# Kernel tuning notes

Hardware: AMD Instinct MI355X
Metric: run time of the kernel (lower is better)

The kernel has to match this reference:

```python
import jax, jax.numpy as jnp
import numpy as np
import math

LN_EPS = 1e-5

def setup_inputs() -> dict:
    key = jax.random.key(0)
    ks = jax.random.split(key, 8)
    B, S, D = 2, 2048, 2048
    sc = 1.0 / math.sqrt(D)
    return {
        "x": jax.random.normal(ks[0], (B, S, D), dtype=jnp.float32),
        "Wq": jax.random.normal(ks[1], (D, D), dtype=jnp.float32) * sc,
        "bq": jnp.zeros((D,), jnp.float32),
        "Wk": jax.random.normal(ks[2], (D, D), dtype=jnp.float32) * sc,
        "bk": jnp.zeros((D,), jnp.float32),
        "Wv": jax.random.normal(ks[3], (D, D), dtype=jnp.float32) * sc,
        "bv": jnp.zeros((D,), jnp.float32),
        "Wo": jax.random.normal(ks[4], (D, D), dtype=jnp.float32) * sc,
        "bo": jnp.zeros((D,), jnp.float32),
        "gamma": jnp.ones((D,), jnp.float32),
        "beta": jnp.zeros((D,), jnp.float32),
        "num_heads": 16,
    }

def reference(x, Wq, bq, Wk, bk, Wv, bv, Wo, bo, gamma, beta, num_heads):
    B, S, D = x.shape
    H = num_heads
    Dh = D // H
    # projections (torch Linear: y = x W^T + b; here W stored as [in,out])
    q = (x @ Wq + bq).reshape(B, S, H, Dh).transpose(0, 2, 1, 3)  # [B,H,S,Dh]
    k = (x @ Wk + bk).reshape(B, S, H, Dh).transpose(0, 2, 1, 3)
    v = (x @ Wv + bv).reshape(B, S, H, Dh).transpose(0, 2, 1, 3)
    scores = jnp.einsum("bhqd,bhkd->bhqk", q, k) / jnp.sqrt(jnp.asarray(Dh, x.dtype))
    causal = jnp.tril(jnp.ones((S, S), bool))  # [S,S]
    scores = jnp.where(causal[None, None], scores, -jnp.inf)
    # original subtracts row-max then softmax == stable softmax
    attn = jax.nn.softmax(scores, axis=-1)
    ctx = jnp.einsum("bhqk,bhkd->bhqd", attn, v)
    ctx = ctx.transpose(0, 2, 1, 3).reshape(B, S, D)
    attn_out = ctx @ Wo + bo
    y = attn_out + x
    mu = jnp.mean(y, axis=-1, keepdims=True)
    var = jnp.mean((y - mu) ** 2, axis=-1, keepdims=True)
    ln = gamma * (y - mu) * jax.lax.rsqrt(var + LN_EPS) + beta
    return (ln, attn_out, k, v)
```

## Files before the change

kernel.cpp:

```cpp
#include <hip/hip_runtime.h>
#include <hip/hip_bf16.h>
#include <math.h>
#include <stdint.h>

typedef __bf16 bf16;
typedef __bf16 bf16x4 __attribute__((ext_vector_type(4)));
typedef __bf16 bf16x8 __attribute__((ext_vector_type(8)));
typedef float f32x4 __attribute__((ext_vector_type(4)));

#define D_MODEL 2048
#define SEQ     2048
#define NHEADS  16
#define DH      128

__device__ __forceinline__ void async_copy16(const bf16* g, bf16* l) {
    typedef const unsigned int __attribute__((address_space(1))) gu32;
    typedef unsigned int __attribute__((address_space(3))) lu32;
    __builtin_amdgcn_global_load_lds((gu32*)g, (lu32*)(unsigned int)(unsigned long long)(l),
                                     16, 0, 0);
}

__global__ __launch_bounds__(256)
void convert_x_kernel(const float* __restrict__ x, bf16* __restrict__ xb)
{
    int i = blockIdx.x * 256 + threadIdx.x;
    float4 v = ((const float4*)x)[i];
    bf16x4 o;
    o[0] = (bf16)v.x; o[1] = (bf16)v.y; o[2] = (bf16)v.z; o[3] = (bf16)v.w;
    ((bf16x4*)xb)[i] = o;
}

__global__ __launch_bounds__(256)
void transpose_w_kernel(const float* __restrict__ Wq, const float* __restrict__ Wk,
                        const float* __restrict__ Wv, const float* __restrict__ Wo,
                        bf16* __restrict__ WTbase)
{
    const int z = blockIdx.z;
    const float* __restrict__ W = (z == 0) ? Wq : (z == 1) ? Wk : (z == 2) ? Wv : Wo;
    bf16* __restrict__ Wt = WTbase + (size_t)z * (D_MODEL * D_MODEL);
    const int n0 = blockIdx.x * 64, k0 = blockIdx.y * 64;
    const int tid = threadIdx.x;
    __shared__ bf16 Tl[64][68];

#pragma unroll
    for (int i = 0; i < 4; ++i) {
        int idx = tid + i * 256;
        int kr = idx >> 4, nc = (idx & 15) * 4;
        float4 w = *(const float4*)&W[(size_t)(k0 + kr) * D_MODEL + n0 + nc];
        Tl[nc + 0][kr] = (bf16)w.x;
        Tl[nc + 1][kr] = (bf16)w.y;
        Tl[nc + 2][kr] = (bf16)w.z;
        Tl[nc + 3][kr] = (bf16)w.w;
    }
    __syncthreads();
#pragma unroll
    for (int i = 0; i < 4; ++i) {
        int idx = tid + i * 256;
        int nr = idx >> 4, kc = (idx & 15) * 4;
        *(bf16x4*)&Wt[(size_t)(n0 + nr) * D_MODEL + k0 + kc] = *(const bf16x4*)&Tl[nr][kc];
    }
}

__global__ __launch_bounds__(256)
void transpose_v_kernel(const float* __restrict__ V, bf16* __restrict__ Vt)
{
    const int s0 = blockIdx.x * 64, d0 = blockIdx.y * 64, bh = blockIdx.z;
    const float* __restrict__ Vb = V + (size_t)bh * SEQ * DH;
    bf16* __restrict__ Vtb = Vt + (size_t)bh * DH * SEQ;
    const int tid = threadIdx.x;
    __shared__ bf16 Tl[64][68];

#pragma unroll
    for (int i = 0; i < 4; ++i) {
        int idx = tid + i * 256;
        int sr = idx >> 4, dc = (idx & 15) * 4;
        float4 v = *(const float4*)&Vb[(size_t)(s0 + sr) * DH + d0 + dc];
        Tl[dc + 0][sr] = (bf16)v.x;
        Tl[dc + 1][sr] = (bf16)v.y;
        Tl[dc + 2][sr] = (bf16)v.z;
        Tl[dc + 3][sr] = (bf16)v.w;
    }
    __syncthreads();
#pragma unroll
    for (int i = 0; i < 4; ++i) {
        int idx = tid + i * 256;
        int dr = idx >> 4, sc = (idx & 15) * 4;
        *(bf16x4*)&Vtb[(size_t)(d0 + dr) * SEQ + s0 + sc] = *(const bf16x4*)&Tl[dr][sc];
    }
}

__device__ __forceinline__ void gemm128_core(const bf16* __restrict__ A,
                                             const bf16* __restrict__ Bt,
                                             int bm, int bn,
                                             int wave, int lane,
                                             bf16* As, bf16* Bs,
                                             f32x4 acc[4][4])
{
    const int l16 = lane & 15, quad = lane >> 4;
    const int wave_m = wave >> 1, wave_n = wave & 1;

    for (int k0 = 0; k0 < D_MODEL; k0 += 64) {
#pragma unroll
        for (int jj = 0; jj < 4; ++jj) {
            int j = wave * 4 + jj;
            int mt = j >> 1, kk = j & 1;
            int col = k0 + kk * 32 + quad * 8;
            const bf16* ga = &A[(size_t)(bm * 128 + mt * 16 + l16) * D_MODEL + col];
            async_copy16(ga, &As[j * 512]);
            const bf16* gb = &Bt[(size_t)(bn * 128 + mt * 16 + l16) * D_MODEL + col];
            async_copy16(gb, &Bs[j * 512]);
        }
        __syncthreads();
#pragma unroll
        for (int kk = 0; kk < 2; ++kk) {
            bf16x8 a[4], b[4];
#pragma unroll
            for (int t = 0; t < 4; ++t) {
                a[t] = *(const bf16x8*)&As[(((wave_m * 4 + t) * 2 + kk) * 64 + lane) * 8];
                b[t] = *(const bf16x8*)&Bs[(((wave_n * 4 + t) * 2 + kk) * 64 + lane) * 8];
            }
#pragma unroll
            for (int t = 0; t < 4; ++t)
#pragma unroll
                for (int t2 = 0; t2 < 4; ++t2)
                    acc[t][t2] = __builtin_amdgcn_mfma_f32_16x16x32_bf16(a[t], b[t2], acc[t][t2], 0, 0, 0);
        }
        __syncthreads();
    }
}

__global__ __launch_bounds__(256)
void gemm_qkv_kernel(const bf16* __restrict__ A, const bf16* __restrict__ WT,
                     const float* __restrict__ bq, const float* __restrict__ bk,
                     const float* __restrict__ bv,
                     bf16* __restrict__ qout, float* __restrict__ kout,
                     bf16* __restrict__ kb16, float* __restrict__ vout)
{
    const int z = blockIdx.z;
    const bf16* __restrict__ Bt = WT + (size_t)z * (D_MODEL * D_MODEL);
    const float* __restrict__ bias = (z == 0) ? bq : (z == 1) ? bk : bv;
    const int bm = blockIdx.y, bn = blockIdx.x;
    const int tid = threadIdx.x;
    const int wave = tid >> 6, lane = tid & 63, quad = lane >> 4, l16 = lane & 15;
    const int wave_m = wave >> 1, wave_n = wave & 1;

    __shared__ bf16 As[8192];
    __shared__ bf16 Bs[8192];
    f32x4 acc[4][4] = {};

    gemm128_core(A, Bt, bm, bn, wave, lane, As, Bs, acc);

#pragma unroll
    for (int t = 0; t < 4; ++t) {
#pragma unroll
        for (int t2 = 0; t2 < 4; ++t2) {
#pragma unroll
            for (int r = 0; r < 4; ++r) {
                int m = bm * 128 + wave_m * 64 + t * 16 + quad * 4 + r;
                int n = bn * 128 + wave_n * 64 + t2 * 16 + l16;
                float val = acc[t][t2][r] + bias[n];
                int b = m >> 11, s = m & (SEQ - 1);
                int h = n >> 7, dh = n & (DH - 1);
                size_t off = ((size_t)(b * NHEADS + h) * SEQ + s) * DH + dh;
                if (z == 0) {
                    qout[off] = (bf16)val;
                } else if (z == 1) {
                    kout[off] = val;
                    kb16[off] = (bf16)val;
                } else {
                    vout[off] = val;
                }
            }
        }
    }
}

__global__ __launch_bounds__(256)
void gemm_out_kernel(const bf16* __restrict__ A, const bf16* __restrict__ Bt,
                     const float* __restrict__ bias, float* __restrict__ out)
{
    const int bm = blockIdx.y, bn = blockIdx.x;
    const int tid = threadIdx.x;
    const int wave = tid >> 6, lane = tid & 63, quad = lane >> 4, l16 = lane & 15;
    const int wave_m = wave >> 1, wave_n = wave & 1;

    __shared__ bf16 As[8192];
    __shared__ bf16 Bs[8192];
    f32x4 acc[4][4] = {};

    gemm128_core(A, Bt, bm, bn, wave, lane, As, Bs, acc);

#pragma unroll
    for (int t = 0; t < 4; ++t) {
#pragma unroll
        for (int t2 = 0; t2 < 4; ++t2) {
#pragma unroll
            for (int r = 0; r < 4; ++r) {
                int m = bm * 128 + wave_m * 64 + t * 16 + quad * 4 + r;
                int n = bn * 128 + wave_n * 64 + t2 * 16 + l16;
                out[(size_t)m * D_MODEL + n] = acc[t][t2][r] + bias[n];
            }
        }
    }
}

__global__ __launch_bounds__(256, 4)
void attn_kernel(const bf16* __restrict__ Q, const bf16* __restrict__ K,
                 const bf16* __restrict__ Vt, bf16* __restrict__ ctx)
{
    const int id = blockIdx.x;
    const int p  = id & 511;
    const int bh = p >> 4;
    const int j  = p & 15;
    const int qb = (id >> 9) ? j : (31 - j);

    const int tid = threadIdx.x;
    const int wave = tid >> 6, lane = tid & 63, quad = lane >> 4, l16 = lane & 15;

    __shared__ bf16 Ks[64 * 128];
    __shared__ bf16 VsT[128 * 64];
    __shared__ bf16 Ps[4 * 16 * 64];
    char* const ksb = (char*)Ks;
    char* const vsb = (char*)VsT;
    char* const psb = (char*)Ps + wave * 2048;

    const bf16* qsrc = Q + ((size_t)bh * SEQ + (size_t)qb * 64 + wave * 16 + l16) * DH;
    bf16x8 qf[4];
#pragma unroll
    for (int dd = 0; dd < 4; ++dd)
        qf[dd] = *(const bf16x8*)&qsrc[dd * 32 + quad * 8];

    f32x4 o[8] = {};
    float m_i[4], l_i[4];
#pragma unroll
    for (int r = 0; r < 4; ++r) { m_i[r] = -INFINITY; l_i[r] = 0.f; }

    const float scale = 0.08838834764831845f;
    const bf16* ksrc0 = K + (size_t)bh * SEQ * DH;
    const bf16* vsrc0 = Vt + (size_t)bh * DH * SEQ;

    for (int kb = 0; kb <= qb; ++kb) {
        __syncthreads();

        {
            const char* kg = (const char*)(ksrc0 + (size_t)(kb * 64) * DH);
#pragma unroll
            for (int i = 0; i < 4; ++i) {
                int seg = i * 4 + wave;
                int row = seg * 4 + (lane >> 4);
                int colb = (lane & 15) * 16;
                const char* src = kg + row * 256 + (colb ^ ((row & 7) << 4));
                async_copy16((const bf16*)src, (bf16*)(ksb + seg * 1024));
            }
            const char* vg = (const char*)(vsrc0 + kb * 64);
#pragma unroll
            for (int i = 0; i < 4; ++i) {
                int seg = i * 4 + wave;
                int d = seg * 8 + (lane >> 3);
                int colb = (lane & 7) * 16;
                const char* src = vg + (size_t)d * (SEQ * 2) + (colb ^ ((d & 7) << 4));
                async_copy16((const bf16*)src, (bf16*)(vsb + seg * 1024));
            }
        }
        __syncthreads();

        float pvals[4][4];
#pragma unroll
        for (int t = 0; t < 4; ++t) {
            f32x4 s = {};
            const int row = t * 16 + l16;
            const int swz = (row & 7) << 4;
#pragma unroll
            for (int dd = 0; dd < 4; ++dd) {
                bf16x8 b = *(const bf16x8*)(ksb + row * 256 + ((dd * 64 + quad * 16) ^ swz));
                s = __builtin_amdgcn_mfma_f32_16x16x32_bf16(qf[dd], b, s, 0, 0, 0);
            }
#pragma unroll
            for (int r = 0; r < 4; ++r) pvals[t][r] = s[r];
        }

        const bool diag = (kb == qb);
#pragma unroll
        for (int r = 0; r < 4; ++r) {
            int qrow = qb * 64 + wave * 16 + quad * 4 + r;
            float mx = -INFINITY;
#pragma unroll
            for (int t = 0; t < 4; ++t) {
                float s = pvals[t][r] * scale;
                int kcol = kb * 64 + t * 16 + l16;
                if (diag && kcol > qrow) s = -INFINITY;
                pvals[t][r] = s;
                mx = fmaxf(mx, s);
            }
#pragma unroll
            for (int off = 1; off < 16; off <<= 1)
                mx = fmaxf(mx, __shfl_xor(mx, off, 64));
            float mnew = fmaxf(m_i[r], mx);
            float alpha = __expf(m_i[r] - mnew);
            m_i[r] = mnew;
            float rs = 0.f;
#pragma unroll
            for (int t = 0; t < 4; ++t) {
                float pexp = __expf(pvals[t][r] - mnew);
                pvals[t][r] = pexp;
                rs += pexp;
            }
#pragma unroll
            for (int off = 1; off < 16; off <<= 1)
                rs += __shfl_xor(rs, off, 64);
            l_i[r] = l_i[r] * alpha + rs;
#pragma unroll
            for (int dt = 0; dt < 8; ++dt) o[dt][r] *= alpha;
        }

#pragma unroll
        for (int t = 0; t < 4; ++t)
#pragma unroll
            for (int r = 0; r < 4; ++r) {
                int row = quad * 4 + r;
                *(bf16*)(psb + row * 128 + (((t * 16 + l16) * 2) ^ ((row & 7) << 4))) =
                    (bf16)pvals[t][r];
            }

        bf16x8 pa[2];
#pragma unroll
        for (int kk2 = 0; kk2 < 2; ++kk2)
            pa[kk2] = *(const bf16x8*)(psb + l16 * 128 +
                                       ((kk2 * 64 + quad * 16) ^ ((l16 & 7) << 4)));
#pragma unroll
        for (int dt = 0; dt < 8; ++dt) {
            const int row = dt * 16 + l16;
            const int swz = (row & 7) << 4;
#pragma unroll
            for (int kk2 = 0; kk2 < 2; ++kk2) {
                bf16x8 b = *(const bf16x8*)(vsb + row * 128 + ((kk2 * 64 + quad * 16) ^ swz));
                o[dt] = __builtin_amdgcn_mfma_f32_16x16x32_bf16(pa[kk2], b, o[dt], 0, 0, 0);
            }
        }
    }

    const int b = bh >> 4, h = bh & (NHEADS - 1);
    float inv_l[4];
#pragma unroll
    for (int r = 0; r < 4; ++r) inv_l[r] = 1.0f / l_i[r];
#pragma unroll
    for (int dt = 0; dt < 8; ++dt) {
#pragma unroll
        for (int r = 0; r < 4; ++r) {
            int s = qb * 64 + wave * 16 + quad * 4 + r;
            int d = dt * 16 + l16;
            ctx[((size_t)(b * SEQ + s)) * D_MODEL + h * DH + d] = (bf16)(o[dt][r] * inv_l[r]);
        }
    }
}

__global__ __launch_bounds__(256)
void ln_kernel(const float* __restrict__ attn, const float* __restrict__ x,
               const float* __restrict__ gamma, const float* __restrict__ beta,
               float* __restrict__ ln)
{
    const int row = blockIdx.x;
    const int tid = threadIdx.x;
    const int wave = tid >> 6, lane = tid & 63;
    const float* a  = attn + (size_t)row * D_MODEL;
    const float* xr = x    + (size_t)row * D_MODEL;

    float4 y4[2];
    float sum = 0.f, sumsq = 0.f;
#pragma unroll
    for (int i = 0; i < 2; ++i) {
        int c = (tid + i * 256) * 4;
        float4 av = *(const float4*)&a[c];
        float4 xv = *(const float4*)&xr[c];
        float4 y;
        y.x = av.x + xv.x; y.y = av.y + xv.y; y.z = av.z + xv.z; y.w = av.w + xv.w;
        y4[i] = y;
        sum   += y.x + y.y + y.z + y.w;
        sumsq += y.x * y.x + y.y * y.y + y.z * y.z + y.w * y.w;
    }
#pragma unroll
    for (int off = 1; off < 64; off <<= 1) {
        sum   += __shfl_xor(sum, off, 64);
        sumsq += __shfl_xor(sumsq, off, 64);
    }
    __shared__ float rsum[4], rsumsq[4];
    if (lane == 0) { rsum[wave] = sum; rsumsq[wave] = sumsq; }
    __syncthreads();
    float tot = 0.f, tot2 = 0.f;
#pragma unroll
    for (int i = 0; i < 4; ++i) { tot += rsum[i]; tot2 += rsumsq[i]; }
    const float mu  = tot * (1.0f / D_MODEL);
    const float var = tot2 * (1.0f / D_MODEL) - mu * mu;
    const float rstd = rsqrtf(var + 1e-5f);

#pragma unroll
    for (int i = 0; i < 2; ++i) {
        int c = (tid + i * 256) * 4;
        float4 gv = *(const float4*)&gamma[c];
        float4 bv = *(const float4*)&beta[c];
        float4 y = y4[i];
        float4 r;
        r.x = gv.x * (y.x - mu) * rstd + bv.x;
        r.y = gv.y * (y.y - mu) * rstd + bv.y;
        r.z = gv.z * (y.z - mu) * rstd + bv.z;
        r.w = gv.w * (y.w - mu) * rstd + bv.w;
        *(float4*)&ln[(size_t)row * D_MODEL + c] = r;
    }
}

extern "C" void kernel_launch(void* const* d_in, const int* in_sizes, int n_in,
                              void* d_out, int out_size, void* d_ws, size_t ws_size,
                              hipStream_t stream)
{
    const float* x     = (const float*)d_in[0];
    const float* Wq    = (const float*)d_in[1];
    const float* bq    = (const float*)d_in[2];
    const float* Wk    = (const float*)d_in[3];
    const float* bk    = (const float*)d_in[4];
    const float* Wv    = (const float*)d_in[5];
    const float* bv    = (const float*)d_in[6];
    const float* Wo    = (const float*)d_in[7];
    const float* bo    = (const float*)d_in[8];
    const float* gamma = (const float*)d_in[9];
    const float* beta  = (const float*)d_in[10];

    float* out      = (float*)d_out;
    float* ln       = out;
    float* attn_out = out + 8388608;
    float* kout     = out + 16777216;
    float* vout     = out + 25165824;

    bf16* wsb  = (bf16*)d_ws;
    bf16* xb   = wsb;
    bf16* WT   = wsb + 8388608;
    bf16* qws  = wsb + 25165824;
    bf16* kb16 = wsb + 33554432;
    bf16* vT   = wsb + 41943040;
    bf16* ctx  = wsb + 50331648;

    convert_x_kernel<<<8192, 256, 0, stream>>>(x, xb);
    transpose_w_kernel<<<dim3(32, 32, 4), 256, 0, stream>>>(Wq, Wk, Wv, Wo, WT);
    gemm_qkv_kernel<<<dim3(16, 32, 3), 256, 0, stream>>>(xb, WT, bq, bk, bv,
                                                          qws, kout, kb16, vout);
    transpose_v_kernel<<<dim3(32, 2, 32), 256, 0, stream>>>(vout, vT);
    attn_kernel<<<dim3(1024), 256, 0, stream>>>(qws, kb16, vT, ctx);
    gemm_out_kernel<<<dim3(16, 32), 256, 0, stream>>>(ctx, WT + 3 * (size_t)(D_MODEL * D_MODEL),
                                                       bo, attn_out);
    ln_kernel<<<4096, 256, 0, stream>>>(attn_out, x, gamma, beta, ln);
}
```

Measured before the change: 637.8 us.

## Replace 128x128 GEMM core with double-buffered 256x256 tile and 8 waves

Replaces the 128x128 tile GEMM, which synchronised around every K-step, with a 256x256 tile computed by 512 threads. It double-buffers LDS and interleaves async global-to-LDS copies for the next K tiles with the MFMA sub-phases, using explicit waitcnt, barriers and setprio. The QKV and output GEMMs move to a 1D grid with a swizzled block order for L2 reuse, and the three QKV weights are treated as one concatenated N dimension. This trades more registers and 128KB of LDS per block for higher arithmetic intensity and overlapped loads. It also brings the risk of a tail effect from fewer blocks (384 and 128) on the GPU.

```diff
diff --git a/kernel.cpp b/kernel.cpp
--- a/kernel.cpp
+++ b/kernel.cpp
@@ -89,78 +89,128 @@
     }
 }
 
-__device__ __forceinline__ void gemm128_core(const bf16* __restrict__ A,
+__device__ __forceinline__ void gemm256_core(const bf16* __restrict__ A,
                                              const bf16* __restrict__ Bt,
                                              int bm, int bn,
-                                             int wave, int lane,
-                                             bf16* As, bf16* Bs,
-                                             f32x4 acc[4][4])
-{
-    const int l16 = lane & 15, quad = lane >> 4;
-    const int wave_m = wave >> 1, wave_n = wave & 1;
-
-    for (int k0 = 0; k0 < D_MODEL; k0 += 64) {
-#pragma unroll
-        for (int jj = 0; jj < 4; ++jj) {
-            int j = wave * 4 + jj;
-            int mt = j >> 1, kk = j & 1;
-            int col = k0 + kk * 32 + quad * 8;
-            const bf16* ga = &A[(size_t)(bm * 128 + mt * 16 + l16) * D_MODEL + col];
-            async_copy16(ga, &As[j * 512]);
-            const bf16* gb = &Bt[(size_t)(bn * 128 + mt * 16 + l16) * D_MODEL + col];
-            async_copy16(gb, &Bs[j * 512]);
-        }
-        __syncthreads();
-#pragma unroll
-        for (int kk = 0; kk < 2; ++kk) {
-            bf16x8 a[4], b[4];
-#pragma unroll
-            for (int t = 0; t < 4; ++t) {
-                a[t] = *(const bf16x8*)&As[(((wave_m * 4 + t) * 2 + kk) * 64 + lane) * 8];
-                b[t] = *(const bf16x8*)&Bs[(((wave_n * 4 + t) * 2 + kk) * 64 + lane) * 8];
-            }
-#pragma unroll
-            for (int t = 0; t < 4; ++t)
-#pragma unroll
-                for (int t2 = 0; t2 < 4; ++t2)
-                    acc[t][t2] = __builtin_amdgcn_mfma_f32_16x16x32_bf16(a[t], b[t2], acc[t][t2], 0, 0, 0);
-        }
-        __syncthreads();
-    }
-}
-
-__global__ __launch_bounds__(256)
+                                             bf16* lds,
+                                             f32x4 acc[8][4])
+{
+    const int tid = threadIdx.x;
+    const int wave = tid >> 6, lane = tid & 63, quad = lane >> 4, l16 = lane & 15;
+    const int wr = wave >> 2, wc = wave & 3;
+    const int rowA = bm * 256, rowB = bn * 256;
+
+    auto stageA = [&](int p, int kt, int h) {
+#pragma unroll
+        for (int j = 0; j < 2; ++j) {
+            const int f = h * 16 + j * 8 + wave;
+            const int mt = f >> 1, kk = f & 1;
+            const bf16* g = &A[(size_t)(rowA + mt * 16 + l16) * D_MODEL + kt * 64 + kk * 32 + quad * 8];
+            async_copy16(g, lds + p * 32768 + f * 512 + lane * 8);
+        }
+    };
+    auto stageB = [&](int p, int kt, int h) {
+#pragma unroll
+        for (int j = 0; j < 2; ++j) {
+            const int f = h * 16 + j * 8 + wave;
+            const int nt = f >> 1, kk = f & 1;
+            const bf16* g = &Bt[(size_t)(rowB + nt * 16 + l16) * D_MODEL + kt * 64 + kk * 32 + quad * 8];
+            async_copy16(g, lds + p * 32768 + 16384 + f * 512 + lane * 8);
+        }
+    };
+
+    stageA(0, 0, 0); stageA(0, 0, 1);
+    stageB(0, 0, 0); stageB(0, 0, 1);
+    stageB(1, 1, 0); stageB(1, 1, 1);
+    asm volatile("s_waitcnt vmcnt(4)" ::: "memory");
+    __builtin_amdgcn_s_barrier();
+
+    for (int t = 0; t < 32; ++t) {
+        const int p = t & 1;
+        const bf16* Ab = lds + p * 32768;
+        const bf16* Bb = Ab + 16384;
+        const int tn1 = (t + 1 < 31) ? t + 1 : 31;
+        const int tn2 = (t + 2 < 31) ? t + 2 : 31;
+        bf16x8 bfr[4][2];
+#pragma unroll
+        for (int q = 0; q < 4; ++q) {
+            bf16x8 af[2][2];
+#pragma unroll
+            for (int mi = 0; mi < 2; ++mi)
+#pragma unroll
+                for (int kk = 0; kk < 2; ++kk) {
+                    const int mt = wr * 8 + 2 * q + mi;
+                    af[mi][kk] = *(const bf16x8*)(Ab + (mt * 2 + kk) * 512 + lane * 8);
+                }
+            if (q == 0) {
+#pragma unroll
+                for (int n = 0; n < 4; ++n)
+#pragma unroll
+                    for (int kk = 0; kk < 2; ++kk) {
+                        const int nt = wc * 4 + n;
+                        bfr[n][kk] = *(const bf16x8*)(Bb + (nt * 2 + kk) * 512 + lane * 8);
+                    }
+                stageA(p ^ 1, tn1, 0);
+            } else if (q == 1) {
+                stageA(p ^ 1, tn1, 1);
+            } else if (q == 2) {
+                stageB(p, tn2, 0);
+            } else {
+                stageB(p, tn2, 1);
+            }
+
+            __builtin_amdgcn_s_barrier();
+            asm volatile("s_waitcnt lgkmcnt(0)" ::: "memory");
+            __builtin_amdgcn_sched_barrier(0);
+            __builtin_amdgcn_s_setprio(1);
+#pragma unroll
+            for (int mi = 0; mi < 2; ++mi)
+#pragma unroll
+                for (int n = 0; n < 4; ++n)
+#pragma unroll
+                    for (int kk = 0; kk < 2; ++kk)
+                        acc[2 * q + mi][n] = __builtin_amdgcn_mfma_f32_16x16x32_bf16(
+                            af[mi][kk], bfr[n][kk], acc[2 * q + mi][n], 0, 0, 0);
+            __builtin_amdgcn_s_setprio(0);
+            if (q == 3) asm volatile("s_waitcnt vmcnt(4)" ::: "memory");
+            __builtin_amdgcn_s_barrier();
+        }
+    }
+    asm volatile("s_waitcnt vmcnt(0)" ::: "memory");
+}
+
+__global__ __launch_bounds__(512, 2)
 void gemm_qkv_kernel(const bf16* __restrict__ A, const bf16* __restrict__ WT,
                      const float* __restrict__ bq, const float* __restrict__ bk,
                      const float* __restrict__ bv,
                      bf16* __restrict__ qout, float* __restrict__ kout,
                      bf16* __restrict__ kb16, float* __restrict__ vout)
 {
-    const int z = blockIdx.z;
-    const bf16* __restrict__ Bt = WT + (size_t)z * (D_MODEL * D_MODEL);
+    __shared__ bf16 lds[65536];
+    const int id = blockIdx.x;
+    const int swz = (id & 7) * 48 + (id >> 3);
+    const int bm = swz / 24, bn = swz % 24;
+
+    f32x4 acc[8][4] = {};
+    gemm256_core(A, WT, bm, bn, lds, acc);
+
+    const int tid = threadIdx.x;
+    const int wave = tid >> 6, lane = tid & 63, quad = lane >> 4, l16 = lane & 15;
+    const int wr = wave >> 2, wc = wave & 3;
+    const int z = bn >> 3;
     const float* __restrict__ bias = (z == 0) ? bq : (z == 1) ? bk : bv;
-    const int bm = blockIdx.y, bn = blockIdx.x;
-    const int tid = threadIdx.x;
-    const int wave = tid >> 6, lane = tid & 63, quad = lane >> 4, l16 = lane & 15;
-    const int wave_m = wave >> 1, wave_n = wave & 1;
-
-    __shared__ bf16 As[8192];
-    __shared__ bf16 Bs[8192];
-    f32x4 acc[4][4] = {};
-
-    gemm128_core(A, Bt, bm, bn, wave, lane, As, Bs, acc);
-
-#pragma unroll
-    for (int t = 0; t < 4; ++t) {
-#pragma unroll
-        for (int t2 = 0; t2 < 4; ++t2) {
+
+#pragma unroll
+    for (int mi = 0; mi < 8; ++mi) {
+#pragma unroll
+        for (int n = 0; n < 4; ++n) {
 #pragma unroll
             for (int r = 0; r < 4; ++r) {
-                int m = bm * 128 + wave_m * 64 + t * 16 + quad * 4 + r;
-                int n = bn * 128 + wave_n * 64 + t2 * 16 + l16;
-                float val = acc[t][t2][r] + bias[n];
+                int m  = bm * 256 + wr * 128 + mi * 16 + quad * 4 + r;
+                int nl = (bn & 7) * 256 + wc * 64 + n * 16 + l16;
+                float val = acc[mi][n][r] + bias[nl];
                 int b = m >> 11, s = m & (SEQ - 1);
-                int h = n >> 7, dh = n & (DH - 1);
+                int h = nl >> 7, dh = nl & (DH - 1);
                 size_t off = ((size_t)(b * NHEADS + h) * SEQ + s) * DH + dh;
                 if (z == 0) {
                     qout[off] = (bf16)val;
@@ -175,30 +225,31 @@
     }
 }
 
-__global__ __launch_bounds__(256)
+__global__ __launch_bounds__(512, 2)
 void gemm_out_kernel(const bf16* __restrict__ A, const bf16* __restrict__ Bt,
                      const float* __restrict__ bias, float* __restrict__ out)
 {
-    const int bm = blockIdx.y, bn = blockIdx.x;
+    __shared__ bf16 lds[65536];
+    const int id = blockIdx.x;
+    const int swz = (id & 7) * 16 + (id >> 3);
+    const int bm = swz >> 3, bn = swz & 7;
+
+    f32x4 acc[8][4] = {};
+    gemm256_core(A, Bt, bm, bn, lds, acc);
+
     const int tid = threadIdx.x;
     const int wave = tid >> 6, lane = tid & 63, quad = lane >> 4, l16 = lane & 15;
-    const int wave_m = wave >> 1, wave_n = wave & 1;
-
-    __shared__ bf16 As[8192];
-    __shared__ bf16 Bs[8192];
-    f32x4 acc[4][4] = {};
-
-    gemm128_core(A, Bt, bm, bn, wave, lane, As, Bs, acc);
-
-#pragma unroll
-    for (int t = 0; t < 4; ++t) {
-#pragma unroll
-        for (int t2 = 0; t2 < 4; ++t2) {
+    const int wr = wave >> 2, wc = wave & 3;
+
+#pragma unroll
+    for (int mi = 0; mi < 8; ++mi) {
+#pragma unroll
+        for (int n = 0; n < 4; ++n) {
 #pragma unroll
             for (int r = 0; r < 4; ++r) {
-                int m = bm * 128 + wave_m * 64 + t * 16 + quad * 4 + r;
-                int n = bn * 128 + wave_n * 64 + t2 * 16 + l16;
-                out[(size_t)m * D_MODEL + n] = acc[t][t2][r] + bias[n];
+                int m = bm * 256 + wr * 128 + mi * 16 + quad * 4 + r;
+                int nn = bn * 256 + wc * 64 + n * 16 + l16;
+                out[(size_t)m * D_MODEL + nn] = acc[mi][n][r] + bias[nn];
             }
         }
     }
@@ -440,11 +491,11 @@
 
     convert_x_kernel<<<8192, 256, 0, stream>>>(x, xb);
     transpose_w_kernel<<<dim3(32, 32, 4), 256, 0, stream>>>(Wq, Wk, Wv, Wo, WT);
-    gemm_qkv_kernel<<<dim3(16, 32, 3), 256, 0, stream>>>(xb, WT, bq, bk, bv,
-                                                          qws, kout, kb16, vout);
+    gemm_qkv_kernel<<<dim3(384), 512, 0, stream>>>(xb, WT, bq, bk, bv,
+                                                    qws, kout, kb16, vout);
     transpose_v_kernel<<<dim3(32, 2, 32), 256, 0, stream>>>(vout, vT);
     attn_kernel<<<dim3(1024), 256, 0, stream>>>(qws, kb16, vT, ctx);
-    gemm_out_kernel<<<dim3(16, 32), 256, 0, stream>>>(ctx, WT + 3 * (size_t)(D_MODEL * D_MODEL),
-                                                       bo, attn_out);
+    gemm_out_kernel<<<dim3(128), 512, 0, stream>>>(ctx, WT + 3 * (size_t)(D_MODEL * D_MODEL),
+                                                    bo, attn_out);
     ln_kernel<<<4096, 256, 0, stream>>>(attn_out, x, gamma, beta, ln);
 }
```

Measured after the change: 582.0 us. 1.1x faster.
